# Performance work log

Measured on AMD Instinct MI355X. Metric: run time of the kernel, lower is better.

## Reference

```python
import jax, jax.numpy as jnp
import numpy as np

B, S, D = 4, 2048, 1024

def setup_inputs() -> dict:
    key = jax.random.key(0)
    kx, kq, kk, kv = jax.random.split(key, 4)
    glorot = (6.0 / (D + D)) ** 0.5
    return {
        "x": jax.random.normal(kx, (B, S, D), dtype=jnp.float32),
        "Wq": jax.random.uniform(kq, (D, D), jnp.float32, -glorot, glorot),
        "Wk": jax.random.uniform(kk, (D, D), jnp.float32, -glorot, glorot),
        "Wv": jax.random.uniform(kv, (D, D), jnp.float32, -glorot, glorot),
    }

def reference(x, Wq, Wk, Wv):
    # q,k,v: [B,S,D]
    q = jnp.einsum("bsd,de->bse", x, Wq)
    k = jnp.einsum("bsd,de->bse", x, Wk)
    v = jnp.einsum("bsd,de->bse", x, Wv)
    scale = jnp.sqrt(jnp.asarray(q.shape[-1], q.dtype))
    scores = jnp.einsum("bqd,bkd->bqk", q, k) / scale  # [B,S,S]
    w = jax.nn.softmax(scores, axis=-1)
    return jnp.einsum("bqk,bkd->bqd", w, v)
```

## Files before the change

kernel.cpp:

```cpp
#include <hip/hip_runtime.h>
#include <hip/hip_bf16.h>


typedef _Float16 half_t;
typedef _Float16 half8 __attribute__((ext_vector_type(8)));
typedef _Float16 half4v __attribute__((ext_vector_type(4)));
typedef float f32x4 __attribute__((ext_vector_type(4)));
typedef float f32x16 __attribute__((ext_vector_type(16)));

__device__ __forceinline__ void load16_to_lds(const half_t* g, half_t* l) {
  __builtin_amdgcn_global_load_lds(
      (const __attribute__((address_space(1))) void*)g,
      (__attribute__((address_space(3))) void*)l, 16, 0, 0);
}

__global__ __launch_bounds__(256, 2) void qkvt_gemm(
    const half_t* __restrict__ xh, const half_t* __restrict__ wt,
    half_t* __restrict__ qk, half_t* __restrict__ vtg) {
  __shared__ __align__(16) half_t As[256 * 64];
  __shared__ __align__(16) half_t Bs[128 * 64];

  constexpr int K = 1024;
  int b = blockIdx.x;
  const half_t* A; const half_t* Bm; half_t* C;
  int lda, ldb, ldc, m0, n0;
  if (b < 512) {
    A = xh; Bm = wt; C = qk; lda = 1024; ldb = 1024; ldc = 2048;
    m0 = (b >> 4) * 256; n0 = (b & 15) * 128;
  } else {
    b -= 512;
    A = wt + (size_t)2 * 1024 * 1024; Bm = xh; C = vtg;
    lda = 1024; ldb = 1024; ldc = 8192;
    m0 = (b >> 6) * 256; n0 = (b & 63) * 128;
  }

  const int t    = threadIdx.x;
  const int wave = t >> 6;
  const int lane = t & 63;
  const int wm   = (wave >> 1) * 128;
  const int wn   = (wave & 1) * 64;
  const int ln   = lane & 31;
  const int hl   = lane >> 5;
  const int lswz = ln & 7;

  const int trow = t >> 3;
  const int tchk = (t & 7) ^ (trow & 7);

  const half_t* gA0 = A  + (size_t)(m0 + trow) * lda + tchk * 8;
  const half_t* gB0 = Bm + (size_t)(n0 + trow) * ldb + tchk * 8;
  const size_t stepA = (size_t)32 * lda;
  const size_t stepB = (size_t)32 * ldb;

  half_t* lA0 = &As[t * 8];
  half_t* lB0 = &Bs[t * 8];

  f32x16 acc[4][2] = {};

  for (int k0 = 0; k0 < K; k0 += 64) {
    __syncthreads();
#pragma unroll
    for (int n = 0; n < 8; ++n)
      load16_to_lds(gA0 + n * stepA + k0, lA0 + n * 2048);
#pragma unroll
    for (int n = 0; n < 4; ++n)
      load16_to_lds(gB0 + n * stepB + k0, lB0 + n * 2048);
    __syncthreads();

#pragma unroll
    for (int kk = 0; kk < 4; ++kk) {
      const int c = kk * 2 + hl;
      half8 a[4], bfr[2];
#pragma unroll
      for (int i = 0; i < 4; ++i)
        a[i] = *(const half8*)&As[(wm + i * 32 + ln) * 64 + (c ^ lswz) * 8];
#pragma unroll
      for (int j = 0; j < 2; ++j)
        bfr[j] = *(const half8*)&Bs[(wn + j * 32 + ln) * 64 + (c ^ lswz) * 8];
#pragma unroll
      for (int i = 0; i < 4; ++i)
#pragma unroll
        for (int j = 0; j < 2; ++j)
          acc[i][j] = __builtin_amdgcn_mfma_f32_32x32x16_f16(a[i], bfr[j], acc[i][j], 0, 0, 0);
    }
  }

#pragma unroll
  for (int i = 0; i < 4; ++i)
#pragma unroll
    for (int j = 0; j < 2; ++j) {
      const int col = n0 + wn + j * 32 + ln;
#pragma unroll
      for (int reg = 0; reg < 16; ++reg) {
        const int row = m0 + wm + i * 32 + 4 * hl + (reg & 3) + 8 * (reg >> 2);
        C[(size_t)row * ldc + col] = (half_t)acc[i][j][reg];
      }
    }
}

__global__ __launch_bounds__(256) void scores_gemm(
    const half_t* __restrict__ qk, half_t* __restrict__ sc,
    float* __restrict__ lpart) {
  __shared__ __align__(16) half_t As[128 * 64];
  __shared__ __align__(16) half_t Bs[128 * 64];

  const int z  = blockIdx.z;
  const int m0 = blockIdx.y * 128;
  const int n0 = blockIdx.x * 128;
  const half_t* A  = qk + (size_t)z * 2048 * 2048;
  const half_t* Bm = A + 1024;
  half_t* C = sc + (size_t)z * 2048 * 2048;
  constexpr int lda = 2048, ldb = 2048, ldc = 2048, K = 1024;

  const int t    = threadIdx.x;
  const int wave = t >> 6;
  const int lane = t & 63;
  const int wm   = (wave >> 1) * 64;
  const int wn   = (wave & 1) * 64;
  const int lm   = lane & 15;
  const int lq   = lane >> 4;
  const int lswz = lm & 7;

  const int trow = t >> 3;
  const int tchk = (t & 7) ^ (trow & 7);

  const half_t* gA0 = A  + (size_t)(m0 + trow) * lda + tchk * 8;
  const half_t* gB0 = Bm + (size_t)(n0 + trow) * ldb + tchk * 8;
  const size_t stepA = (size_t)32 * lda;
  const size_t stepB = (size_t)32 * ldb;

  half_t* lA0 = &As[t * 8];
  half_t* lB0 = &Bs[t * 8];

  f32x4 acc[4][4] = {};

  for (int k0 = 0; k0 < K; k0 += 64) {
    __syncthreads();
#pragma unroll
    for (int n = 0; n < 4; ++n) {
      load16_to_lds(gA0 + n * stepA + k0, lA0 + n * 2048);
      load16_to_lds(gB0 + n * stepB + k0, lB0 + n * 2048);
    }
    __syncthreads();

#pragma unroll
    for (int kk = 0; kk < 2; ++kk) {
      const int pos = ((kk * 4 + lq) ^ lswz) * 8;
      half8 a[4], bf[4];
#pragma unroll
      for (int i = 0; i < 4; ++i)
        a[i] = *(const half8*)&As[(wm + i * 16 + lm) * 64 + pos];
#pragma unroll
      for (int j = 0; j < 4; ++j)
        bf[j] = *(const half8*)&Bs[(wn + j * 16 + lm) * 64 + pos];
#pragma unroll
      for (int i = 0; i < 4; ++i)
#pragma unroll
        for (int j = 0; j < 4; ++j)
          acc[i][j] = __builtin_amdgcn_mfma_f32_16x16x32_f16(a[i], bf[j], acc[i][j], 0, 0, 0);
    }
  }

  const float scale = 1.0f / 32.0f;
#pragma unroll
  for (int i = 0; i < 4; ++i)
#pragma unroll
    for (int r = 0; r < 4; ++r) {
      const int row = m0 + wm + i * 16 + lq * 4 + r;
      float s = 0.f;
#pragma unroll
      for (int j = 0; j < 4; ++j) {
        const int col = n0 + wn + j * 16 + lm;
        float v = __expf(acc[i][j][r] * scale - 8.0f);
        s += v;
        C[(size_t)row * ldc + col] = (half_t)v;
      }
      s += __shfl_xor(s, 1); s += __shfl_xor(s, 2);
      s += __shfl_xor(s, 4); s += __shfl_xor(s, 8);
      if (lm == 0)
        lpart[((size_t)z * 2048 + row) * 32 + blockIdx.x * 2 + (wave & 1)] = s;
    }
}

__global__ __launch_bounds__(256) void pv_gemm(
    const half_t* __restrict__ sc, const half_t* __restrict__ vtg,
    float* __restrict__ out, const float* __restrict__ lpart) {
  __shared__ __align__(16) half_t As[128 * 64];
  __shared__ __align__(16) half_t Bs[128 * 64];
  __shared__ float linv[128];

  const int z  = blockIdx.z;
  const int m0 = blockIdx.x * 128;
  const int n0 = blockIdx.y * 128;
  const half_t* A  = sc  + (size_t)z * 2048 * 2048;
  const half_t* Bm = vtg + (size_t)z * 2048;
  float* C = out + (size_t)z * 2048 * 1024;
  constexpr int lda = 2048, ldb = 8192, ldc = 1024, K = 2048;

  const int t    = threadIdx.x;
  const int wave = t >> 6;
  const int lane = t & 63;
  const int wm   = (wave >> 1) * 64;
  const int wn   = (wave & 1) * 64;
  const int lm   = lane & 15;
  const int lq   = lane >> 4;
  const int lswz = lm & 7;

  if (t < 128) {
    const float4* lp = (const float4*)&lpart[((size_t)z * 2048 + m0 + t) * 32];
    float s = 0.f;
#pragma unroll
    for (int p = 0; p < 8; ++p) {
      float4 v = lp[p];
      s += v.x + v.y + v.z + v.w;
    }
    linv[t] = 1.0f / s;
  }

  const int trow = t >> 3;
  const int tchk = (t & 7) ^ (trow & 7);

  const half_t* gA0 = A  + (size_t)(m0 + trow) * lda + tchk * 8;
  const half_t* gB0 = Bm + (size_t)(n0 + trow) * ldb + tchk * 8;
  const size_t stepA = (size_t)32 * lda;
  const size_t stepB = (size_t)32 * ldb;

  half_t* lA0 = &As[t * 8];
  half_t* lB0 = &Bs[t * 8];

  f32x4 acc[4][4] = {};

  for (int k0 = 0; k0 < K; k0 += 64) {
    __syncthreads();
#pragma unroll
    for (int n = 0; n < 4; ++n) {
      load16_to_lds(gA0 + n * stepA + k0, lA0 + n * 2048);
      load16_to_lds(gB0 + n * stepB + k0, lB0 + n * 2048);
    }
    __syncthreads();

#pragma unroll
    for (int kk = 0; kk < 2; ++kk) {
      const int pos = ((kk * 4 + lq) ^ lswz) * 8;
      half8 a[4], bf[4];
#pragma unroll
      for (int i = 0; i < 4; ++i)
        a[i] = *(const half8*)&As[(wm + i * 16 + lm) * 64 + pos];
#pragma unroll
      for (int j = 0; j < 4; ++j)
        bf[j] = *(const half8*)&Bs[(wn + j * 16 + lm) * 64 + pos];
#pragma unroll
      for (int i = 0; i < 4; ++i)
#pragma unroll
        for (int j = 0; j < 4; ++j)
          acc[i][j] = __builtin_amdgcn_mfma_f32_16x16x32_f16(a[i], bf[j], acc[i][j], 0, 0, 0);
    }
  }

#pragma unroll
  for (int i = 0; i < 4; ++i)
#pragma unroll
    for (int r = 0; r < 4; ++r) {
      const int lrow = wm + i * 16 + lq * 4 + r;
      const float inv = linv[lrow];
      const int row = m0 + lrow;
#pragma unroll
      for (int j = 0; j < 4; ++j) {
        const int col = n0 + wn + j * 16 + lm;
        C[(size_t)row * ldc + col] = acc[i][j][r] * inv;
      }
    }
}

__global__ __launch_bounds__(256) void prep(
    const float* __restrict__ x, half_t* __restrict__ xh,
    const float* __restrict__ Wq, const float* __restrict__ Wk,
    const float* __restrict__ Wv, half_t* __restrict__ wt) {
  __shared__ half_t tile[32][33];
  const int b = blockIdx.x;
  const int t = threadIdx.x;
  if (b < 8192) {
    const int i = (b * 256 + t) * 4;
    const float4 v = *reinterpret_cast<const float4*>(x + i);
    half4v o;
    o.x = (half_t)v.x; o.y = (half_t)v.y; o.z = (half_t)v.z; o.w = (half_t)v.w;
    *reinterpret_cast<half4v*>(xh + i) = o;
  } else {
    int bb = b - 8192;
    const int w = bb >> 10; bb &= 1023;
    const float* in = (w == 0) ? Wq : (w == 1) ? Wk : Wv;
    half_t* o = wt + (size_t)w * 1024 * 1024;
    const int r0 = (bb >> 5) * 32, c0 = (bb & 31) * 32;
    const int tx = t & 31, ty = t >> 5;
#pragma unroll
    for (int i = 0; i < 32; i += 8)
      tile[ty + i][tx] = (half_t)in[(size_t)(r0 + ty + i) * 1024 + c0 + tx];
    __syncthreads();
#pragma unroll
    for (int i = 0; i < 32; i += 8)
      o[(size_t)(c0 + ty + i) * 1024 + r0 + tx] = tile[tx][ty + i];
  }
}

extern "C" void kernel_launch(void* const* d_in, const int* in_sizes, int n_in,
                              void* d_out, int out_size, void* d_ws, size_t ws_size,
                              hipStream_t stream) {
  constexpr int Bb = 4, S = 2048, D = 1024;
  constexpr size_t MS = (size_t)Bb * S;

  const float* x  = (const float*)d_in[0];
  const float* Wq = (const float*)d_in[1];
  const float* Wk = (const float*)d_in[2];
  const float* Wv = (const float*)d_in[3];
  float* out = (float*)d_out;

  char* p = (char*)d_ws;
  half_t* xh    = (half_t*)p; p += MS * D * 2;
  half_t* wt    = (half_t*)p; p += (size_t)3 * D * D * 2;
  half_t* qk    = (half_t*)p; p += MS * (size_t)(2 * D) * 2;
  half_t* vtg   = (half_t*)p; p += (size_t)D * MS * 2;
  half_t* sc    = (half_t*)p; p += (size_t)Bb * S * S * 2;
  float*  lpart = (float*)p;  p += MS * 32 * 4;

  prep<<<11264, 256, 0, stream>>>(x, xh, Wq, Wk, Wv, wt);
  qkvt_gemm<<<768, 256, 0, stream>>>(xh, wt, qk, vtg);
  scores_gemm<<<dim3(16, 16, Bb), 256, 0, stream>>>(qk, sc, lpart);
  pv_gemm<<<dim3(16, 8, Bb), 256, 0, stream>>>(sc, vtg, out, lpart);
}
```

Measured before the change: 248.7 us.

## Rewrite QKV projection GEMM as 8-wave 256x256 double-buffered pipelined kernel

Replaces the 256x128 single-buffered QKV projection GEMM with a 512-thread, 256x256-tile kernel. It double-buffers A and B in LDS and interleaves global-to-LDS loads with MFMA quadrants under explicit waitcnt and barriers, using s_setprio around the MFMA blocks. It also switches from 32x32x16 to 16x16x32 MFMA. The aim is to hide memory latency and raise data reuse per tile. In exchange it uses 128KB of LDS per block, which limits occupancy, and adds many barriers whose hand-written waitcnt logic is fragile.

After: 242.6 us. -2.5%, faster.

```diff
diff --git a/kernel.cpp b/kernel.cpp
--- a/kernel.cpp
+++ b/kernel.cpp
@@ -6,7 +6,6 @@
 typedef _Float16 half8 __attribute__((ext_vector_type(8)));
 typedef _Float16 half4v __attribute__((ext_vector_type(4)));
 typedef float f32x4 __attribute__((ext_vector_type(4)));
-typedef float f32x16 __attribute__((ext_vector_type(16)));
 
 __device__ __forceinline__ void load16_to_lds(const half_t* g, half_t* l) {
   __builtin_amdgcn_global_load_lds(
@@ -14,87 +13,154 @@
       (__attribute__((address_space(3))) void*)l, 16, 0, 0);
 }
 
-__global__ __launch_bounds__(256, 2) void qkvt_gemm(
+__global__ __launch_bounds__(512, 2) void qkvt_gemm8(
     const half_t* __restrict__ xh, const half_t* __restrict__ wt,
     half_t* __restrict__ qk, half_t* __restrict__ vtg) {
-  __shared__ __align__(16) half_t As[256 * 64];
-  __shared__ __align__(16) half_t Bs[128 * 64];
-
-  constexpr int K = 1024;
+  __shared__ __align__(16) half_t As[2][256 * 64];
+  __shared__ __align__(16) half_t Bs[2][256 * 64];
+
   int b = blockIdx.x;
   const half_t* A; const half_t* Bm; half_t* C;
-  int lda, ldb, ldc, m0, n0;
-  if (b < 512) {
-    A = xh; Bm = wt; C = qk; lda = 1024; ldb = 1024; ldc = 2048;
-    m0 = (b >> 4) * 256; n0 = (b & 15) * 128;
+  int ldc, m0, n0;
+  if (b < 256) {
+    A = xh; Bm = wt; C = qk; ldc = 2048;
+    m0 = (b >> 3) * 256; n0 = (b & 7) * 256;
   } else {
-    b -= 512;
-    A = wt + (size_t)2 * 1024 * 1024; Bm = xh; C = vtg;
-    lda = 1024; ldb = 1024; ldc = 8192;
-    m0 = (b >> 6) * 256; n0 = (b & 63) * 128;
-  }
-
-  const int t    = threadIdx.x;
-  const int wave = t >> 6;
-  const int lane = t & 63;
-  const int wm   = (wave >> 1) * 128;
-  const int wn   = (wave & 1) * 64;
-  const int ln   = lane & 31;
-  const int hl   = lane >> 5;
-  const int lswz = ln & 7;
+    b -= 256;
+    A = wt + (size_t)2 * 1024 * 1024; Bm = xh; C = vtg; ldc = 8192;
+    m0 = (b >> 5) * 256; n0 = (b & 31) * 256;
+  }
+
+  const int t     = threadIdx.x;
+  const int lane  = t & 63;
+  const int wave  = t >> 6;
+  const int wr128 = (wave >> 2) * 128;
+  const int wc64  = (wave & 3) * 64;
+  const int lm    = lane & 15;
+  const int lq    = lane >> 4;
+  const int pos0  = (lq ^ (lm & 7)) * 8;
+  const int pos1  = ((4 + lq) ^ (lm & 7)) * 8;
+  const int t8    = t * 8;
 
   const int trow = t >> 3;
   const int tchk = (t & 7) ^ (trow & 7);
-
-  const half_t* gA0 = A  + (size_t)(m0 + trow) * lda + tchk * 8;
-  const half_t* gB0 = Bm + (size_t)(n0 + trow) * ldb + tchk * 8;
-  const size_t stepA = (size_t)32 * lda;
-  const size_t stepB = (size_t)32 * ldb;
-
-  half_t* lA0 = &As[t * 8];
-  half_t* lB0 = &Bs[t * 8];
-
-  f32x16 acc[4][2] = {};
-
-  for (int k0 = 0; k0 < K; k0 += 64) {
-    __syncthreads();
-#pragma unroll
-    for (int n = 0; n < 8; ++n)
-      load16_to_lds(gA0 + n * stepA + k0, lA0 + n * 2048);
-#pragma unroll
-    for (int n = 0; n < 4; ++n)
-      load16_to_lds(gB0 + n * stepB + k0, lB0 + n * 2048);
-    __syncthreads();
-
-#pragma unroll
-    for (int kk = 0; kk < 4; ++kk) {
-      const int c = kk * 2 + hl;
-      half8 a[4], bfr[2];
-#pragma unroll
-      for (int i = 0; i < 4; ++i)
-        a[i] = *(const half8*)&As[(wm + i * 32 + ln) * 64 + (c ^ lswz) * 8];
-#pragma unroll
-      for (int j = 0; j < 2; ++j)
-        bfr[j] = *(const half8*)&Bs[(wn + j * 32 + ln) * 64 + (c ^ lswz) * 8];
-#pragma unroll
-      for (int i = 0; i < 4; ++i)
-#pragma unroll
-        for (int j = 0; j < 2; ++j)
-          acc[i][j] = __builtin_amdgcn_mfma_f32_32x32x16_f16(a[i], bfr[j], acc[i][j], 0, 0, 0);
-    }
-  }
-
-#pragma unroll
-  for (int i = 0; i < 4; ++i)
-#pragma unroll
-    for (int j = 0; j < 2; ++j) {
-      const int col = n0 + wn + j * 32 + ln;
-#pragma unroll
-      for (int reg = 0; reg < 16; ++reg) {
-        const int row = m0 + wm + i * 32 + 4 * hl + (reg & 3) + 8 * (reg >> 2);
-        C[(size_t)row * ldc + col] = (half_t)acc[i][j][reg];
+  const half_t* gA0 = A  + (size_t)(m0 + trow) * 1024 + tchk * 8;
+  const half_t* gB0 = Bm + (size_t)(n0 + trow) * 1024 + tchk * 8;
+
+  f32x4 acc[8][4] = {};
+  half8 va[4][2], vb0[2][2], vb1[2][2];
+
+#define ST_A(buf, h, kt) do {                                                  \
+    load16_to_lds(gA0 + (size_t)((h)*128) * 1024 + (size_t)(kt) * 64,          \
+                  &As[buf][(h)*128*64] + t8);                                  \
+    load16_to_lds(gA0 + (size_t)((h)*128+64) * 1024 + (size_t)(kt) * 64,       \
+                  &As[buf][((h)*128+64)*64] + t8);                             \
+  } while (0)
+#define ST_B(buf, h, kt) do {                                                  \
+    load16_to_lds(gB0 + (size_t)((h)*128) * 1024 + (size_t)(kt) * 64,          \
+                  &Bs[buf][(h)*128*64] + t8);                                  \
+    load16_to_lds(gB0 + (size_t)((h)*128+64) * 1024 + (size_t)(kt) * 64,       \
+                  &Bs[buf][((h)*128+64)*64] + t8);                             \
+  } while (0)
+#define RD_A(buf, mh) do {                                                     \
+    _Pragma("unroll") for (int m = 0; m < 4; ++m) {                            \
+      const int ar = wr128 + (mh)*64 + m * 16 + lm;                            \
+      va[m][0] = *(const half8*)&As[buf][ar * 64 + pos0];                      \
+      va[m][1] = *(const half8*)&As[buf][ar * 64 + pos1];                      \
+    } } while (0)
+#define RD_B(buf, nh, vb) do {                                                 \
+    _Pragma("unroll") for (int n = 0; n < 2; ++n) {                            \
+      const int br = wc64 + (nh)*32 + n * 16 + lm;                             \
+      vb[n][0] = *(const half8*)&Bs[buf][br * 64 + pos0];                      \
+      vb[n][1] = *(const half8*)&Bs[buf][br * 64 + pos1];                      \
+    } } while (0)
+#define MF_Q(mh, nh, vb) do {                                                  \
+    _Pragma("unroll") for (int kk = 0; kk < 2; ++kk)                           \
+    _Pragma("unroll") for (int m = 0; m < 4; ++m)                              \
+    _Pragma("unroll") for (int n = 0; n < 2; ++n)                              \
+      acc[(mh)*4+m][(nh)*2+n] = __builtin_amdgcn_mfma_f32_16x16x32_f16(        \
+          va[m][kk], vb[n][kk], acc[(mh)*4+m][(nh)*2+n], 0, 0, 0);             \
+  } while (0)
+#define LGKM0 asm volatile("s_waitcnt lgkmcnt(0)" ::: "memory")
+#define BAR   __builtin_amdgcn_s_barrier()
+#define PRIO1 __builtin_amdgcn_s_setprio(1)
+#define PRIO0 __builtin_amdgcn_s_setprio(0)
+
+  ST_A(0, 0, 0); ST_A(0, 1, 0);
+  ST_B(0, 0, 0); ST_B(0, 1, 0);
+  ST_B(1, 0, 1); ST_B(1, 1, 1);
+  asm volatile("s_waitcnt vmcnt(4)" ::: "memory");
+  BAR;
+
+#pragma unroll 1
+  for (int i = 0; i < 8; ++i) {
+    const int st1 = (2 * i + 1 < 15) ? 2 * i + 1 : 15;
+    const int st2 = (2 * i + 2 < 15) ? 2 * i + 2 : 15;
+    const int st3 = (2 * i + 3 < 15) ? 2 * i + 3 : 15;
+    RD_A(0, 0); RD_B(0, 0, vb0);
+    ST_A(1, 0, st1);
+    asm volatile("s_waitcnt lgkmcnt(8)" ::: "memory");
+    BAR; LGKM0;
+    PRIO1; MF_Q(0, 0, vb0); PRIO0;
+    BAR;
+    RD_B(0, 1, vb1);
+    ST_A(1, 1, st1);
+    BAR; LGKM0;
+    PRIO1; MF_Q(0, 1, vb1); PRIO0;
+    BAR;
+    RD_A(0, 1);
+    ST_B(0, 0, st2);
+    BAR; LGKM0;
+    PRIO1; MF_Q(1, 0, vb0); PRIO0;
+    BAR;
+    ST_B(0, 1, st2);
+    BAR; LGKM0;
+    PRIO1; MF_Q(1, 1, vb1); PRIO0;
+    asm volatile("s_waitcnt vmcnt(4)" ::: "memory");
+    BAR;
+    RD_A(1, 0); RD_B(1, 0, vb0);
+    ST_A(0, 0, st2);
+    asm volatile("s_waitcnt lgkmcnt(8)" ::: "memory");
+    BAR; LGKM0;
+    PRIO1; MF_Q(0, 0, vb0); PRIO0;
+    BAR;
+    RD_B(1, 1, vb1);
+    ST_A(0, 1, st2);
+    BAR; LGKM0;
+    PRIO1; MF_Q(0, 1, vb1); PRIO0;
+    BAR;
+    RD_A(1, 1);
+    ST_B(1, 0, st3);
+    BAR; LGKM0;
+    PRIO1; MF_Q(1, 0, vb0); PRIO0;
+    BAR;
+    ST_B(1, 1, st3);
+    BAR; LGKM0;
+    PRIO1; MF_Q(1, 1, vb1); PRIO0;
+    asm volatile("s_waitcnt vmcnt(4)" ::: "memory");
+    BAR;
+  }
+
+#pragma unroll
+  for (int m = 0; m < 8; ++m)
+#pragma unroll
+    for (int n = 0; n < 4; ++n) {
+      const int col = n0 + wc64 + n * 16 + lm;
+#pragma unroll
+      for (int r = 0; r < 4; ++r) {
+        const int row = m0 + wr128 + m * 16 + lq * 4 + r;
+        C[(size_t)row * ldc + col] = (half_t)acc[m][n][r];
       }
     }
+#undef ST_A
+#undef ST_B
+#undef RD_A
+#undef RD_B
+#undef MF_Q
+#undef LGKM0
+#undef BAR
+#undef PRIO1
+#undef PRIO0
 }
 
 __global__ __launch_bounds__(256) void scores_gemm(
@@ -322,7 +388,7 @@
   float*  lpart = (float*)p;  p += MS * 32 * 4;
 
   prep<<<11264, 256, 0, stream>>>(x, xh, Wq, Wk, Wv, wt);
-  qkvt_gemm<<<768, 256, 0, stream>>>(xh, wt, qk, vtg);
+  qkvt_gemm8<<<384, 512, 0, stream>>>(xh, wt, qk, vtg);
   scores_gemm<<<dim3(16, 16, Bb), 256, 0, stream>>>(qk, sc, lpart);
   pv_gemm<<<dim3(16, 8, Bb), 256, 0, stream>>>(sc, vtg, out, lpart);
 }
```
